# Kernel tuning notes

Hardware: AMD Instinct MI355X
Metric: run time of the kernel (lower is better)

## Reference

```python
import jax, jax.numpy as jnp
import numpy as np

# Model dims (match init_kwargs / input_specs)
L = 2      # layer_dim
B = 64     # batch
T = 512    # max seq len
D = 256    # input_dim (== hidden_dim, required by stacked wiring)
H = 256    # hidden_dim
O = 2      # output_dim


def setup_inputs() -> dict:
    key = jax.random.key(0)
    ks = jax.random.split(key, 10)
    s = 1.0 / np.sqrt(H)
    f32 = jnp.float32
    return {
        "x_data": jax.random.normal(ks[0], (B, T, D), f32),
        "x_length": jax.random.randint(ks[1], (B,), 1, T + 1),
        "x_label": jax.random.uniform(ks[2], (B,), f32),
        # Per-layer GRU-cell weights, stacked over layers (bias=False).
        "Wz": (jax.random.normal(ks[3], (L, D, H), f32) * s),
        "Uz": (jax.random.normal(ks[4], (L, H, H), f32) * s),
        "Wr": (jax.random.normal(ks[5], (L, D, H), f32) * s),
        "Ur": (jax.random.normal(ks[6], (L, H, H), f32) * s),
        "Wh": (jax.random.normal(ks[7], (L, D, H), f32) * s),
        "Uh": (jax.random.normal(ks[8], (L, H, H), f32) * s),
        # Output projection of the last layer (only last layer's `out` is used).
        "Wo": (jax.random.normal(ks[9], (H, O), f32) * s),
    }


def reference(x_data, x_length, x_label, Wz, Uz, Wr, Ur, Wh, Uh, Wo):
    # Training-mode forward: sum over batch and valid timesteps of
    # (label - sigmoid(out[:, 1]))**2, with per-layer states S1, S2
    # carried across time. Vectorized over batch; lax.scan over time.
    Tn = x_data.shape[1]
    xs = jnp.swapaxes(x_data, 0, 1)  # [T, B, D]
    S1_0 = jnp.zeros((L, B, H), x_data.dtype)
    S2_0 = jnp.zeros((L, B, H), x_data.dtype)

    def step(carry, xt):
        S1, S2 = carry
        inp = xt  # [B, D]
        for l in range(L):  # small fixed layer loop
            z = jax.nn.sigmoid(inp @ Wz[l] + S1[l] @ Uz[l])
            r = jax.nn.sigmoid(inp @ Wr[l] + S1[l] @ Ur[l])
            h = jnp.tanh(inp @ Wh[l] + (r * S1[l]) @ Uh[l])
            hn = (1.0 - z) * S1[l] + z * h          # new hidden (S1)
            S2n = z * S2[l] + (1.0 - z) * h          # secondary memory (S2)
            S1 = S1.at[l].set(hn)
            S2 = S2.at[l].set(S2n)
            inp = hn
        score = jax.nn.sigmoid((inp @ Wo)[:, 1])     # out[:, 1] -> [B]
        return (S1, S2), score

    _, scores = jax.lax.scan(step, (S1_0, S2_0), xs)  # [T, B]
    mask = (jnp.arange(Tn)[:, None] < x_length[None, :]).astype(scores.dtype)
    loss = jnp.sum(mask * (x_label[None, :] - scores) ** 2)
    return loss
```

## Files before the change

### kernel.cpp

```cpp
#include <hip/hip_runtime.h>

#define LAY 2
#define BATCH 64
#define TMAX 512
#define DIM 256
#define AST 264
#define CHUNK 16

typedef float floatx4 __attribute__((ext_vector_type(4)));
typedef __bf16 bf16x8 __attribute__((ext_vector_type(8)));
#define MFMA_FP8  __builtin_amdgcn_mfma_f32_16x16x32_fp8_fp8
#define MFMA_BF16 __builtin_amdgcn_mfma_f32_16x16x32_bf16

#define BAR_LDS() asm volatile("s_waitcnt lgkmcnt(0)\n\ts_barrier" ::: "memory")

#define OFF_WPW 0xA0000
#define OFF_FLG 0x150000
#define OFF_XP  0x200000
#define OFF_HP  0x1C00000
#define OFF_HN  0x3600000

__device__ __forceinline__ unsigned short f2bf(float f) {
    unsigned int u = __float_as_uint(f);
    unsigned int r = u + 0x7fffu + ((u >> 16) & 1u);
    return (unsigned short)(r >> 16);
}
__device__ __forceinline__ unsigned int pk2(float a, float b) {
    return (unsigned int)__builtin_amdgcn_cvt_pk_fp8_f32(a, b, 0, false);
}
__device__ __forceinline__ unsigned char f2q(float a) { return (unsigned char)(pk2(a, a) & 0xff); }
__device__ __forceinline__ void unp4(unsigned int u, float* f) {
    auto lo = __builtin_amdgcn_cvt_pk_f32_fp8((int)u, false);
    auto hi = __builtin_amdgcn_cvt_pk_f32_fp8((int)u, true);
    f[0] = lo[0]; f[1] = lo[1]; f[2] = hi[0]; f[3] = hi[1];
}
__device__ __forceinline__ float sigf(float x) {
    return __builtin_amdgcn_rcpf(1.f + __expf(-x));
}
__device__ __forceinline__ float tanhfast2y(float twoy) { return 2.f * sigf(twoy) - 1.f; }

__device__ __forceinline__ void ast_u32(unsigned int* p, unsigned int v) {
    __hip_atomic_store(p, v, __ATOMIC_RELAXED, __HIP_MEMORY_SCOPE_AGENT);
}

__device__ __forceinline__ long quant8(const float* s) {
    unsigned int p01 = pk2(8.f * s[0 * 256], 8.f * s[1 * 256]);
    unsigned int p23 = pk2(8.f * s[2 * 256], 8.f * s[3 * 256]);
    unsigned int p45 = pk2(8.f * s[4 * 256], 8.f * s[5 * 256]);
    unsigned int p67 = pk2(8.f * s[6 * 256], 8.f * s[7 * 256]);
    unsigned long long v = (unsigned long long)(p01 & 0xffffu)
                         | ((unsigned long long)(p23 & 0xffffu) << 16)
                         | ((unsigned long long)(p45 & 0xffffu) << 32)
                         | ((unsigned long long)(p67 & 0xffffu) << 48);
    return (long)v;
}

__global__ void prep_weights(const float* __restrict__ Wz, const float* __restrict__ Wr,
                             const float* __restrict__ Wh,
                             unsigned char* __restrict__ ws, float* __restrict__ out) {
    int T = blockIdx.x * 256 + threadIdx.x;
    if (T == 0) out[0] = 0.f;
    if (T < 192) ((int*)(ws + OFF_FLG))[T] = 0;
    int e = T & 3, lane = (T >> 2) & 63;
    int kf = (T >> 8) & 7, nt = (T >> 11) & 15, mw = T >> 15;
    const float* s = (mw == 0 ? Wz : mw == 1 ? Wr : Wh);
    int n  = nt * 16 + (lane & 15);
    int k0 = kf * 32 + (lane >> 4) * 8 + 2 * e;
    unsigned int v = (unsigned int)f2bf(s[(k0 << 8) + n]) |
                     ((unsigned int)f2bf(s[((k0 + 1) << 8) + n]) << 16);
    int addr = ((mw * 16 + nt) * 8 + kf) * 1024 + lane * 16 + 4 * e;
    *(unsigned int*)(ws + OFF_WPW + addr) = v;
}

template <int SCORE, int WMODE, int POST>
__device__ __forceinline__ void scan_body(
    const unsigned int* __restrict__ xp,
    const float* __restrict__ Uzs, const float* __restrict__ Urs,
    const float* __restrict__ Uhs,
    int bg, unsigned char* __restrict__ hnout,
    const int* __restrict__ xlen, const float* __restrict__ xlab,
    const float* __restrict__ Wo, float* __restrict__ out,
    int* wflags, int* pflag,
    unsigned char (*s1q)[AST], unsigned char (*rsq)[AST], float (*s1o)[264],
    float* wo1s, int* s_rdy, int tmax)
{
    const int tid = threadIdx.x, wave = tid >> 6, lane = tid & 63;
    const int l15 = lane & 15, quad = lane >> 4;
    const int b0 = bg * 16;

    for (int i = tid; i < 16 * AST; i += 1024) ((unsigned char*)s1q)[i] = 0;
    if (SCORE && tid < DIM) wo1s[tid] = Wo[2 * tid + 1];
    const int lenr = xlen[b0 + l15];
    const float labr = SCORE ? xlab[b0 + l15] : 0.f;
    (void)lenr; (void)labr;

    const int nt = wave;
    const int colA = nt * 16 + l15, rowb = quad * 4;

    long uz[8], ur[8], uh[8];
    {
        const int nb = nt * 16 + l15;
#pragma unroll
        for (int kf = 0; kf < 8; ++kf) {
            const size_t kb = (size_t)(kf * 32 + quad * 8) * 256 + nb;
            uz[kf] = quant8(Uzs + kb);
            ur[kf] = quant8(Urs + kb);
            uh[kf] = quant8(Uhs + kb);
        }
    }
    float s1r[4] = {};
    float accl = 0.f;
    int ready = 0;
    __syncthreads();

    for (int t = 0; t < tmax; ++t) {
        if constexpr (WMODE == 1) {
            if (t >= ready) {
                if (tid == 0) {
                    int vv, g = 0;
                    for (;;) {
                        vv = 1 << 30;
#pragma unroll
                        for (int q = 0; q < 4; ++q) {
                            int m = __hip_atomic_load(wflags + q, __ATOMIC_RELAXED, __HIP_MEMORY_SCOPE_AGENT);
                            vv = m < vv ? m : vv;
                        }
                        if (vv > t || ++g > (1 << 19)) break;
                        __builtin_amdgcn_s_sleep(2);
                    }
                    __threadfence();
                    *s_rdy = vv > t ? vv : t + 1;
                }
                __syncthreads();
                ready = *s_rdy;
            }
        } else if constexpr (WMODE == 2) {
            if (t >= ready) {
                if (tid == 0) {
                    const int ch = t >> 4;
                    int g = 0;
                    for (;;) {
                        int c = __hip_atomic_load(wflags + ch, __ATOMIC_RELAXED, __HIP_MEMORY_SCOPE_AGENT);
                        if (c >= 16 || ++g > (1 << 19)) break;
                        __builtin_amdgcn_s_sleep(2);
                    }
                    int ch2 = ch + 1;
                    while (ch2 < TMAX / CHUNK &&
                           __hip_atomic_load(wflags + ch2, __ATOMIC_RELAXED,
                                             __HIP_MEMORY_SCOPE_AGENT) >= 16) ++ch2;
                    __threadfence();
                    *s_rdy = ch2 * CHUNK;
                }
                __syncthreads();
                ready = *s_rdy;
            }
        }

        const unsigned int* xpt = xp + ((size_t)(bg * 512 + t) * 1024 + nt * 64 + lane) * 3;
        unsigned int xz = xpt[0];
        unsigned int xr = xpt[1];
        unsigned int xh = xpt[2];

        long sf[8];
#pragma unroll
        for (int kf = 0; kf < 8; ++kf) sf[kf] = *(const long*)&s1q[l15][kf * 32 + quad * 8];
        floatx4 zer = {0.f, 0.f, 0.f, 0.f};
        floatx4 ra0 = zer, ra1 = zer, za0 = zer, za1 = zer;
#pragma unroll
        for (int kf = 0; kf < 4; ++kf) {
            ra0 = MFMA_FP8(sf[kf],     ur[kf],     ra0, 0, 0, 0);
            ra1 = MFMA_FP8(sf[kf + 4], ur[kf + 4], ra1, 0, 0, 0);
            za0 = MFMA_FP8(sf[kf],     uz[kf],     za0, 0, 0, 0);
            za1 = MFMA_FP8(sf[kf + 4], uz[kf + 4], za1, 0, 0, 0);
        }
        floatx4 ra = ra0 + ra1;
        float xrf[4];
        unp4(xr, xrf);
#pragma unroll
        for (int i = 0; i < 4; ++i) {
            float r = sigf(0.125f * ra[i] + 0.0625f * xrf[i]);
            rsq[rowb + i][colA] = f2q(r * s1r[i]);
        }
        BAR_LDS();

        long rf[8];
#pragma unroll
        for (int kf = 0; kf < 8; ++kf) rf[kf] = *(const long*)&rsq[l15][kf * 32 + quad * 8];
        floatx4 ha0 = zer, ha1 = zer;
#pragma unroll
        for (int kf = 0; kf < 4; ++kf) {
            ha0 = MFMA_FP8(rf[kf],     uh[kf],     ha0, 0, 0, 0);
            ha1 = MFMA_FP8(rf[kf + 4], uh[kf + 4], ha1, 0, 0, 0);
        }
        floatx4 ha = ha0 + ha1;
        floatx4 za = za0 + za1;
        float xzf[4], xhf[4];
        unp4(xz, xzf); unp4(xh, xhf);
#pragma unroll
        for (int i = 0; i < 4; ++i) {
            float z = sigf(0.125f * za[i] + 0.0625f * xzf[i]);
            float h = tanhfast2y(0.25f * ha[i] + 0.125f * xhf[i]);
            float hn = fmaf(z, h - s1r[i], s1r[i]);
            s1r[i] = hn;
            s1q[rowb + i][colA] = f2q(hn);
            if (SCORE) s1o[rowb + i][colA] = hn;
        }
        BAR_LDS();

        if (!SCORE) {
            const int r = tid >> 6, c = (tid & 63) * 4;
            unsigned int v4 = *(const unsigned int*)&s1q[r][c];
            *(unsigned int*)(hnout + ((size_t)(b0 + r) * 512 + t) * 256 + c) = v4;
        } else if (wave == 0) {
            const int row = l15, c0 = quad * 64;
            float p = 0.f;
#pragma unroll
            for (int u = 0; u < 64; u += 4) {
                float4 sv = *(const float4*)&s1o[row][c0 + u];
                float4 wv = *(const float4*)&wo1s[c0 + u];
                p = fmaf(sv.x, wv.x, p); p = fmaf(sv.y, wv.y, p);
                p = fmaf(sv.z, wv.z, p); p = fmaf(sv.w, wv.w, p);
            }
            p += __shfl_xor(p, 16);
            p += __shfl_xor(p, 32);
            if (lane < 16 && t < lenr) {
                float sc = sigf(p);
                float d = labr - sc;
                accl = fmaf(d, d, accl);
            }
        }

        if (POST && (((t & (CHUNK - 1)) == (CHUNK - 1)) || t == tmax - 1)) {
            __syncthreads();
            if (tid == 0) {
                __threadfence();
                __hip_atomic_store(pflag, t + 1, __ATOMIC_RELEASE, __HIP_MEMORY_SCOPE_AGENT);
            }
        }
    }

    if (SCORE && wave == 0) {
        accl += __shfl_xor(accl, 1);
        accl += __shfl_xor(accl, 2);
        accl += __shfl_xor(accl, 4);
        accl += __shfl_xor(accl, 8);
        if (lane == 0) atomicAdd(out, accl);
    }
}

__global__ __launch_bounds__(1024, 4) void fused_pipeline(
    const float* __restrict__ x,
    unsigned int* __restrict__ XP, unsigned int* __restrict__ HP,
    const unsigned char* __restrict__ wpW, unsigned char* __restrict__ HN,
    const int* __restrict__ xlen, const float* __restrict__ xlab,
    const float* __restrict__ Wo, float* __restrict__ out, int* flags,
    const float* __restrict__ Uz, const float* __restrict__ Ur,
    const float* __restrict__ Uh,
    const float* __restrict__ Wz, const float* __restrict__ Wr,
    const float* __restrict__ Wh)
{
    __shared__ __align__(16) unsigned char s1q[16][AST];
    __shared__ __align__(16) unsigned char rsq[16][AST];
    __shared__ __align__(16) float s1o[16][264];
    __shared__ float wo1s[DIM];
    __shared__ int s_rdy;
    __shared__ __align__(16) unsigned int xpstage[3072];

    const int bid = blockIdx.x;
    const int tid = threadIdx.x, wave = tid >> 6, lane = tid & 63;
    const int l15 = lane & 15, quad = lane >> 4;
    int* cnt = flags + 32;

    if (bid >= 24) {
        const int idx = bid - 24;
        const int pt = idx & 511, pbg = idx >> 9;
        const float* s = x + ((size_t)(pbg * 16 + l15) * 512 + pt) * 256;
        bf16x8 af[8];
#pragma unroll
        for (int kf = 0; kf < 8; ++kf) {
            float4 a = *(const float4*)(s + kf * 32 + quad * 8);
            float4 b = *(const float4*)(s + kf * 32 + quad * 8 + 4);
            union { unsigned short u[8]; bf16x8 v; } cv;
            cv.u[0] = f2bf(a.x); cv.u[1] = f2bf(a.y); cv.u[2] = f2bf(a.z); cv.u[3] = f2bf(a.w);
            cv.u[4] = f2bf(b.x); cv.u[5] = f2bf(b.y); cv.u[6] = f2bf(b.z); cv.u[7] = f2bf(b.w);
            af[kf] = cv.v;
        }
        floatx4 az = {0.f, 0.f, 0.f, 0.f}, ar = az, ah = az;
        const unsigned char* bz = wpW + (size_t)((0 * 16 + wave) * 8) * 1024 + lane * 16;
        const unsigned char* br = wpW + (size_t)((1 * 16 + wave) * 8) * 1024 + lane * 16;
        const unsigned char* bh = wpW + (size_t)((2 * 16 + wave) * 8) * 1024 + lane * 16;
#pragma unroll
        for (int kf = 0; kf < 8; ++kf) {
            az = MFMA_BF16(af[kf], *(const bf16x8*)(bz + kf * 1024), az, 0, 0, 0);
            ar = MFMA_BF16(af[kf], *(const bf16x8*)(br + kf * 1024), ar, 0, 0, 0);
            ah = MFMA_BF16(af[kf], *(const bf16x8*)(bh + kf * 1024), ah, 0, 0, 0);
        }
        xpstage[tid * 3 + 0] = pk2(16.f * az[0], 16.f * az[1]) | (pk2(16.f * az[2], 16.f * az[3]) << 16);
        xpstage[tid * 3 + 1] = pk2(16.f * ar[0], 16.f * ar[1]) | (pk2(16.f * ar[2], 16.f * ar[3]) << 16);
        xpstage[tid * 3 + 2] = pk2(16.f * ah[0], 16.f * ah[1]) | (pk2(16.f * ah[2], 16.f * ah[3]) << 16);
        __syncthreads();
        const size_t base3 = (size_t)(pbg * 512 + pt) * 3072;
        ast_u32(&XP[base3 + tid],        xpstage[tid]);
        ast_u32(&XP[base3 + 1024 + tid], xpstage[1024 + tid]);
        ast_u32(&XP[base3 + 2048 + tid], xpstage[2048 + tid]);
        __syncthreads();
        if (tid == 0)
            __hip_atomic_fetch_add(cnt + pbg * 32 + (pt >> 4), 1,
                                   __ATOMIC_RELAXED, __HIP_MEMORY_SCOPE_AGENT);
        return;
    }

    int role, bg, p = 0;
    if (bid < 4)       { role = 0; bg = bid; }
    else if (bid < 20) { role = 1; bg = (bid - 4) >> 2; p = (bid - 4) & 3; }
    else               { role = 2; bg = bid - 20; }
    const int b0 = bg * 16;

    int v = xlen[b0 + l15];
#pragma unroll
    for (int o = 1; o < 16; o <<= 1) v = max(v, __shfl_xor(v, o));
    const int tmax = __builtin_amdgcn_readfirstlane(v);

    if (role == 0) {
        scan_body<0, 2, 1>(XP, Uz, Ur, Uh, bg, HN, xlen, xlab, Wo, out,
                           cnt + bg * 32, flags + bg, s1q, rsq, s1o, wo1s, &s_rdy, tmax);
    } else if (role == 2) {
        scan_body<1, 1, 0>(HP, Uz + 65536, Ur + 65536, Uh + 65536, bg, nullptr,
                           xlen, xlab, Wo, out,
                           flags + 4 + bg * 4, nullptr, s1q, rsq, s1o, wo1s, &s_rdy, tmax);
    } else {
        int* wf = flags + bg;
        int* pf = flags + 4 + bg * 4 + p;
        const int nt = wave;
        long wz1[8], wr1[8], wh1[8];
        {
            const int nb = nt * 16 + l15;
#pragma unroll
            for (int kf = 0; kf < 8; ++kf) {
                const size_t kb = (size_t)(kf * 32 + quad * 8) * 256 + nb;
                wz1[kf] = quant8(Wz + 65536 + kb);
                wr1[kf] = quant8(Wr + 65536 + kb);
                wh1[kf] = quant8(Wh + 65536 + kb);
            }
        }
        for (int base = 0; base < tmax; base += CHUNK) {
            const int target = (base + CHUNK < tmax) ? base + CHUNK : tmax;
            if (tid == 0) {
                int vv, g = 0;
                for (;;) {
                    vv = __hip_atomic_load(wf, __ATOMIC_RELAXED, __HIP_MEMORY_SCOPE_AGENT);
                    if (vv >= target || ++g > (1 << 19)) break;
                    __builtin_amdgcn_s_sleep(2);
                }
                __threadfence();
            }
            __syncthreads();

            const int t0 = base + p * 4;
            const int t1 = (t0 + 4 < tmax) ? t0 + 4 : tmax;
            for (int t = t0; t < t1; ++t) {
                const unsigned char* sA = HN + ((size_t)(b0 + l15) * 512 + t) * 256;
                long af[8];
#pragma unroll
                for (int kf = 0; kf < 8; ++kf) af[kf] = *(const long*)(sA + kf * 32 + quad * 8);
                floatx4 az = {0.f, 0.f, 0.f, 0.f}, ar = az, ah = az;
#pragma unroll
                for (int kf = 0; kf < 8; ++kf) {
                    az = MFMA_FP8(af[kf], wz1[kf], az, 0, 0, 0);
                    ar = MFMA_FP8(af[kf], wr1[kf], ar, 0, 0, 0);
                    ah = MFMA_FP8(af[kf], wh1[kf], ah, 0, 0, 0);
                }
                const size_t ob3 = ((size_t)(bg * 512 + t) * 1024 + nt * 64 + lane) * 3;
                HP[ob3 + 0] = pk2(2.f * az[0], 2.f * az[1]) | (pk2(2.f * az[2], 2.f * az[3]) << 16);
                HP[ob3 + 1] = pk2(2.f * ar[0], 2.f * ar[1]) | (pk2(2.f * ar[2], 2.f * ar[3]) << 16);
                HP[ob3 + 2] = pk2(2.f * ah[0], 2.f * ah[1]) | (pk2(2.f * ah[2], 2.f * ah[3]) << 16);
            }

            __syncthreads();
            if (tid == 0) {
                __threadfence();
                __hip_atomic_store(pf, base + CHUNK, __ATOMIC_RELEASE, __HIP_MEMORY_SCOPE_AGENT);
            }
        }
    }
}

extern "C" void kernel_launch(void* const* d_in, const int* in_sizes, int n_in,
                              void* d_out, int out_size, void* d_ws, size_t ws_size,
                              hipStream_t stream) {
    const float* x    = (const float*)d_in[0];
    const int*   xlen = (const int*)d_in[1];
    const float* xlab = (const float*)d_in[2];
    const float* Wz   = (const float*)d_in[3];
    const float* Uz   = (const float*)d_in[4];
    const float* Wr   = (const float*)d_in[5];
    const float* Ur   = (const float*)d_in[6];
    const float* Wh   = (const float*)d_in[7];
    const float* Uh   = (const float*)d_in[8];
    const float* Wo   = (const float*)d_in[9];
    float* out = (float*)d_out;

    unsigned char* ws  = (unsigned char*)d_ws;
    unsigned char* wpW = ws + OFF_WPW;
    int*           FLG = (int*)(ws + OFF_FLG);
    unsigned int*  XP  = (unsigned int*)(ws + OFF_XP);
    unsigned int*  HP  = (unsigned int*)(ws + OFF_HP);
    unsigned char* HN  = ws + OFF_HN;

    prep_weights<<<384, 256, 0, stream>>>(Wz, Wr, Wh, ws, out);
    fused_pipeline<<<2072, 1024, 0, stream>>>(x, XP, HP, wpW, HN,
                                              xlen, xlab, Wo, out, FLG,
                                              Uz, Ur, Uh, Wz, Wr, Wh);
}
```

Baseline: 1.081 ms.

## Drop weight-prep kernel, convert W on the fly, parallelize score dot product

Removes the separate prep_weights launch. The projection blocks now read fp32 Wz/Wr/Wh directly and convert them to bf16 inside the MFMA loop, and flags and output are cleared with hipMemsetAsync. The score computation moves from a single wave doing 64-element partial dots to all 16 waves each handling one batch row with a full-wave shuffle reduction, with a per-wave atomicAdd at the end. This trades a launch and a prep pass for strided uncoalesced fp32 weight loads repeated by every projection block, plus 16 atomics per block instead of one.

```diff
diff --git a/kernel.cpp b/kernel.cpp
--- a/kernel.cpp
+++ b/kernel.cpp
@@ -14,7 +14,6 @@
 
 #define BAR_LDS() asm volatile("s_waitcnt lgkmcnt(0)\n\ts_barrier" ::: "memory")
 
-#define OFF_WPW 0xA0000
 #define OFF_FLG 0x150000
 #define OFF_XP  0x200000
 #define OFF_HP  0x1C00000
@@ -53,23 +52,6 @@
                          | ((unsigned long long)(p45 & 0xffffu) << 32)
                          | ((unsigned long long)(p67 & 0xffffu) << 48);
     return (long)v;
-}
-
-__global__ void prep_weights(const float* __restrict__ Wz, const float* __restrict__ Wr,
-                             const float* __restrict__ Wh,
-                             unsigned char* __restrict__ ws, float* __restrict__ out) {
-    int T = blockIdx.x * 256 + threadIdx.x;
-    if (T == 0) out[0] = 0.f;
-    if (T < 192) ((int*)(ws + OFF_FLG))[T] = 0;
-    int e = T & 3, lane = (T >> 2) & 63;
-    int kf = (T >> 8) & 7, nt = (T >> 11) & 15, mw = T >> 15;
-    const float* s = (mw == 0 ? Wz : mw == 1 ? Wr : Wh);
-    int n  = nt * 16 + (lane & 15);
-    int k0 = kf * 32 + (lane >> 4) * 8 + 2 * e;
-    unsigned int v = (unsigned int)f2bf(s[(k0 << 8) + n]) |
-                     ((unsigned int)f2bf(s[((k0 + 1) << 8) + n]) << 16);
-    int addr = ((mw * 16 + nt) * 8 + kf) * 1024 + lane * 16 + 4 * e;
-    *(unsigned int*)(ws + OFF_WPW + addr) = v;
 }
 
 template <int SCORE, int WMODE, int POST>
@@ -90,9 +72,8 @@
 
     for (int i = tid; i < 16 * AST; i += 1024) ((unsigned char*)s1q)[i] = 0;
     if (SCORE && tid < DIM) wo1s[tid] = Wo[2 * tid + 1];
-    const int lenr = xlen[b0 + l15];
-    const float labr = SCORE ? xlab[b0 + l15] : 0.f;
-    (void)lenr; (void)labr;
+    const int lenw = SCORE ? xlen[b0 + wave] : 0;
+    const float labw = SCORE ? xlab[b0 + wave] : 0.f;
 
     const int nt = wave;
     const int colA = nt * 16 + l15, rowb = quad * 4;
@@ -211,21 +192,18 @@
             const int r = tid >> 6, c = (tid & 63) * 4;
             unsigned int v4 = *(const unsigned int*)&s1q[r][c];
             *(unsigned int*)(hnout + ((size_t)(b0 + r) * 512 + t) * 256 + c) = v4;
-        } else if (wave == 0) {
-            const int row = l15, c0 = quad * 64;
-            float p = 0.f;
-#pragma unroll
-            for (int u = 0; u < 64; u += 4) {
-                float4 sv = *(const float4*)&s1o[row][c0 + u];
-                float4 wv = *(const float4*)&wo1s[c0 + u];
-                p = fmaf(sv.x, wv.x, p); p = fmaf(sv.y, wv.y, p);
-                p = fmaf(sv.z, wv.z, p); p = fmaf(sv.w, wv.w, p);
-            }
-            p += __shfl_xor(p, 16);
-            p += __shfl_xor(p, 32);
-            if (lane < 16 && t < lenr) {
+        } else {
+            float4 sv = *(const float4*)&s1o[wave][lane * 4];
+            float4 wv = *(const float4*)&wo1s[lane * 4];
+            float p = sv.x * wv.x;
+            p = fmaf(sv.y, wv.y, p);
+            p = fmaf(sv.z, wv.z, p);
+            p = fmaf(sv.w, wv.w, p);
+#pragma unroll
+            for (int o = 1; o < 64; o <<= 1) p += __shfl_xor(p, o);
+            if (lane == 0 && t < lenw) {
                 float sc = sigf(p);
-                float d = labr - sc;
+                float d = labw - sc;
                 accl = fmaf(d, d, accl);
             }
         }
@@ -239,19 +217,13 @@
         }
     }
 
-    if (SCORE && wave == 0) {
-        accl += __shfl_xor(accl, 1);
-        accl += __shfl_xor(accl, 2);
-        accl += __shfl_xor(accl, 4);
-        accl += __shfl_xor(accl, 8);
-        if (lane == 0) atomicAdd(out, accl);
-    }
+    if (SCORE && lane == 0) atomicAdd(out, accl);
 }
 
 __global__ __launch_bounds__(1024, 4) void fused_pipeline(
     const float* __restrict__ x,
     unsigned int* __restrict__ XP, unsigned int* __restrict__ HP,
-    const unsigned char* __restrict__ wpW, unsigned char* __restrict__ HN,
+    unsigned char* __restrict__ HN,
     const int* __restrict__ xlen, const float* __restrict__ xlab,
     const float* __restrict__ Wo, float* __restrict__ out, int* flags,
     const float* __restrict__ Uz, const float* __restrict__ Ur,
@@ -286,14 +258,21 @@
             af[kf] = cv.v;
         }
         floatx4 az = {0.f, 0.f, 0.f, 0.f}, ar = az, ah = az;
-        const unsigned char* bz = wpW + (size_t)((0 * 16 + wave) * 8) * 1024 + lane * 16;
-        const unsigned char* br = wpW + (size_t)((1 * 16 + wave) * 8) * 1024 + lane * 16;
-        const unsigned char* bh = wpW + (size_t)((2 * 16 + wave) * 8) * 1024 + lane * 16;
+        const int n = wave * 16 + l15;
 #pragma unroll
         for (int kf = 0; kf < 8; ++kf) {
-            az = MFMA_BF16(af[kf], *(const bf16x8*)(bz + kf * 1024), az, 0, 0, 0);
-            ar = MFMA_BF16(af[kf], *(const bf16x8*)(br + kf * 1024), ar, 0, 0, 0);
-            ah = MFMA_BF16(af[kf], *(const bf16x8*)(bh + kf * 1024), ah, 0, 0, 0);
+            const int kbase = (kf * 32 + quad * 8) << 8;
+            union { unsigned short u[8]; bf16x8 v; } cz, cr, chh;
+#pragma unroll
+            for (int j = 0; j < 8; ++j) {
+                const int o = kbase + (j << 8) + n;
+                cz.u[j]  = f2bf(Wz[o]);
+                cr.u[j]  = f2bf(Wr[o]);
+                chh.u[j] = f2bf(Wh[o]);
+            }
+            az = MFMA_BF16(af[kf], cz.v,  az, 0, 0, 0);
+            ar = MFMA_BF16(af[kf], cr.v,  ar, 0, 0, 0);
+            ah = MFMA_BF16(af[kf], chh.v, ah, 0, 0, 0);
         }
         xpstage[tid * 3 + 0] = pk2(16.f * az[0], 16.f * az[1]) | (pk2(16.f * az[2], 16.f * az[3]) << 16);
         xpstage[tid * 3 + 1] = pk2(16.f * ar[0], 16.f * ar[1]) | (pk2(16.f * ar[2], 16.f * ar[3]) << 16);
@@ -401,14 +380,14 @@
     float* out = (float*)d_out;
 
     unsigned char* ws  = (unsigned char*)d_ws;
-    unsigned char* wpW = ws + OFF_WPW;
     int*           FLG = (int*)(ws + OFF_FLG);
     unsigned int*  XP  = (unsigned int*)(ws + OFF_XP);
     unsigned int*  HP  = (unsigned int*)(ws + OFF_HP);
     unsigned char* HN  = ws + OFF_HN;
 
-    prep_weights<<<384, 256, 0, stream>>>(Wz, Wr, Wh, ws, out);
-    fused_pipeline<<<2072, 1024, 0, stream>>>(x, XP, HP, wpW, HN,
+    hipMemsetAsync(FLG, 0, 192 * sizeof(int), stream);
+    hipMemsetAsync(out, 0, sizeof(float), stream);
+    fused_pipeline<<<2072, 1024, 0, stream>>>(x, XP, HP, HN,
                                               xlen, xlab, Wo, out, FLG,
                                               Uz, Ur, Uh, Wz, Wr, Wh);
 }
```

Measured after the change: 1.182 ms. +9.3%, slower.
